# Kernel tuning notes

Hardware: AMD Instinct MI355X
Metric: run time of the kernel (lower is better)

## Reference

```python
import jax, jax.numpy as jnp
import numpy as np

FEATURES = 4096
BATCH = 2048


def setup_inputs() -> dict:
    key = jax.random.key(0)
    kx, kk = jax.random.split(key)
    x = jax.random.normal(kx, (BATCH, FEATURES), dtype=jnp.float32)
    kernel = jax.random.normal(kk, (FEATURES,), dtype=jnp.float32)
    return {"x": x, "kernel": kernel}


def reference(x, kernel):
    n = kernel.shape[0]
    i = jnp.arange(n)[:, None]   # [n,1]
    j = jnp.arange(n)[None, :]   # [1,n]
    idx = i - j                   # Toeplitz offsets
    # W[i,j] = kernel[i-j] if i>=j else 0  (causal lower-triangular Toeplitz)
    W = jnp.where(idx >= 0, kernel[jnp.clip(idx, 0, n - 1)], 0.0)
    # out[b,i] = sum_{j<=i} x[b,j] * kernel[i-j]  == x @ W.T
    return x @ W.T
```

## Files before the change

kernel.cpp:

```cpp
#include <hip/hip_runtime.h>
#include <hip/hip_bf16.h>


typedef unsigned short u16;
typedef __attribute__((ext_vector_type(8))) short  bf16x8;
typedef __attribute__((ext_vector_type(8))) unsigned short u16x8;
typedef __attribute__((ext_vector_type(4))) float  f32x4;

#define KDIM 4096
#define NDIM 4096
#define MDIM 2048
#define KREV_STRIDE 4608
#define KREV_BYTES  (8 * KREV_STRIDE * 2)
#define BSTRIDE 520

static __device__ inline u16 f2bf(float f) {
  unsigned u = __builtin_bit_cast(unsigned, f);
  unsigned r = u + 0x7FFFu + ((u >> 16) & 1u);
  return (u16)(r >> 16);
}

static __device__ inline void async_copy16(const void* g, void* l) {
  __builtin_amdgcn_global_load_lds((const __attribute__((address_space(1))) void*)g,
                                   (__attribute__((address_space(3))) void*)l,
                                   16, 0, 0);
}

__global__ __launch_bounds__(256) void prep(const float* __restrict__ x,
                                            const float* __restrict__ kern,
                                            u16* __restrict__ xb,
                                            u16* __restrict__ krevs,
                                            int conv_blocks) {
  int kb = (int)blockIdx.x - conv_blocks;
  if (kb >= 0) {
    int u = kb * 256 + threadIdx.x;
    for (int a = 0; a < 8; ++a) {
      int t = u + a - 8;
      u16 v = 0;
      if (t >= 0 && t <= 4095) v = f2bf(kern[4095 - t]);
      krevs[a * KREV_STRIDE + u] = v;
    }
  } else {
    size_t i = ((size_t)blockIdx.x * 256 + threadIdx.x) * 8;
    const f32x4* p = (const f32x4*)(x + i);
    f32x4 v0 = p[0], v1 = p[1];
    u16x8 r;
    r[0] = f2bf(v0[0]); r[1] = f2bf(v0[1]); r[2] = f2bf(v0[2]); r[3] = f2bf(v0[3]);
    r[4] = f2bf(v1[0]); r[5] = f2bf(v1[1]); r[6] = f2bf(v1[2]); r[7] = f2bf(v1[3]);
    *(u16x8*)(xb + i) = r;
  }
}

template <bool CONV>
__global__ __launch_bounds__(512, 4) void toeplitz_gemm(const void* __restrict__ Av,
                                                        const u16* __restrict__ krevs,
                                                        float* __restrict__ out) {
  __shared__ __align__(16) char smem_raw[49408];
  u16*   A_all = (u16*)smem_raw;
  u16*   B_all = (u16*)(smem_raw + 32768);
  f32x4* ep    = (f32x4*)smem_raw;

  const int tid  = threadIdx.x;
  const int w    = tid >> 6;
  const int g    = w >> 2;
  const int wl   = w & 3;
  const int lane = tid & 63;
  const int lane16 = lane & 15;
  const int quad   = lane >> 4;
  const int wm = wl >> 1;
  const int wn = wl & 1;

  const int b    = (int)blockIdx.x;
  const int rank = (b < 256) ? b : 511 - (b & 255);
  const int ct   = 31 - (rank >> 4);
  const int n0   = ct * 128;
  const int m0   = (rank & 15) * 128;
  const int W    = 3968 - n0;

  int boff[4];
  for (int fn = 0; fn < 4; ++fn) {
    int n_g = n0 + wn * 64 + fn * 16 + lane16;
    int s0  = 4095 - n_g + quad * 8;
    int a   = s0 & 7;
    boff[fn] = a * BSTRIDE + (s0 - a + 8 - W);
  }

  f32x4 acc[4][4] = {};
  const int srow8 = lane >> 3;
  const int ssrc  = ((lane & 7) ^ srow8) * 8;

  const u16*  xb = (const u16*)Av;
  const float* xf = (const float*)Av;
  u16* A_g = A_all + g * 8192;

  auto stageA = [&](int t) {
    const int k0 = t * 128 + g * 64;
    if constexpr (CONV) {
      int j    = tid & 255;
      int row  = j >> 1;
      int lh   = j & 1;
      for (int lc = 0; lc < 4; ++lc) {
        int l = lh * 4 + lc;
        int p = l ^ (row & 7);
        const f32x4* px = (const f32x4*)(xf + (size_t)(m0 + row) * KDIM + k0 + l * 8);
        f32x4 v0 = px[0], v1 = px[1];
        u16x8 r;
        r[0]=f2bf(v0[0]); r[1]=f2bf(v0[1]); r[2]=f2bf(v0[2]); r[3]=f2bf(v0[3]);
        r[4]=f2bf(v1[0]); r[5]=f2bf(v1[1]); r[6]=f2bf(v1[2]); r[7]=f2bf(v1[3]);
        *(u16x8*)(&A_g[row * 64 + p * 8]) = r;
      }
    } else {
      for (int c = 0; c < 4; ++c) {
        int g8  = c * 4 + wl;
        int row = g8 * 8 + srow8;
        async_copy16(xb + (size_t)(m0 + row) * KDIM + k0 + ssrc,
                     &A_g[g8 * 512]);
      }
    }
  };
  auto stageB = [&](int c) {
    async_copy16(krevs + w * KREV_STRIDE + W + c * 256 + (lane << 3),
                 &B_all[(c & 1) * 4160 + w * BSTRIDE]);
  };

  stageB(0);
  stageA(0);

  const int cmax = ct >> 1;
  for (int t = 0; ; ++t) {
    __syncthreads();
    const u16* Bb  = B_all + ((t >> 1) & 1) * 4160;
    const int  ksl = (t & 1) * 128 + g * 64;
    for (int kk = 0; kk < 2; ++kk) {
      bf16x8 af[4];
      const int p = (kk * 4 + quad) ^ (lane16 & 7);
      for (int fm = 0; fm < 4; ++fm) {
        int row = wm * 64 + fm * 16 + lane16;
        af[fm] = *(const bf16x8*)(&A_g[row * 64 + p * 8]);
      }
      bf16x8 bf[4];
      for (int fn = 0; fn < 4; ++fn)
        bf[fn] = *(const bf16x8*)(&Bb[boff[fn] + ksl + kk * 32]);
      for (int fm = 0; fm < 4; ++fm)
        for (int fn = 0; fn < 4; ++fn)
          acc[fm][fn] = __builtin_amdgcn_mfma_f32_16x16x32_bf16(af[fm], bf[fn], acc[fm][fn], 0, 0, 0);
    }
    if (t == ct) break;
    __syncthreads();
    stageA(t + 1);
    if (!(t & 1) && ((t >> 1) + 1) <= cmax) stageB((t >> 1) + 1);
  }

  const int j = tid & 255;
  for (int r = 0; r < 2; ++r) {
    __syncthreads();
    if (g == 1) {
      for (int fm2 = 0; fm2 < 2; ++fm2)
        for (int fn = 0; fn < 4; ++fn)
          ep[j * 9 + fm2 * 4 + fn] = acc[r * 2 + fm2][fn];
    }
    __syncthreads();
    if (g == 0) {
      for (int fm2 = 0; fm2 < 2; ++fm2)
        for (int fn = 0; fn < 4; ++fn)
          acc[r * 2 + fm2][fn] += ep[j * 9 + fm2 * 4 + fn];
    }
  }

  if (g == 0) {
    for (int fm = 0; fm < 4; ++fm) {
      int row_base = m0 + wm * 64 + fm * 16 + quad * 4;
      for (int fn = 0; fn < 4; ++fn) {
        int col = n0 + wn * 64 + fn * 16 + lane16;
        for (int r = 0; r < 4; ++r)
          out[(size_t)(row_base + r) * NDIM + col] = acc[fm][fn][r];
      }
    }
  }
}

extern "C" void kernel_launch(void* const* d_in, const int* in_sizes, int n_in,
                              void* d_out, int out_size, void* d_ws, size_t ws_size,
                              hipStream_t stream) {
  const float* x    = (const float*)d_in[0];
  const float* kern = (const float*)d_in[1];
  float* out = (float*)d_out;

  u16* krevs = (u16*)d_ws;
  u16* xb    = (u16*)((char*)d_ws + KREV_BYTES);
  const size_t need_fast = (size_t)KREV_BYTES + (size_t)MDIM * KDIM * 2;

  if (ws_size >= need_fast) {
    prep<<<4096 + 18, 256, 0, stream>>>(x, kern, xb, krevs, 4096);
    toeplitz_gemm<false><<<512, 512, 0, stream>>>(xb, krevs, out);
  } else {
    prep<<<18, 256, 0, stream>>>(x, kern, xb, krevs, 0);
    toeplitz_gemm<true><<<512, 512, 0, stream>>>(x, krevs, out);
  }
}
```

Baseline: 125.9 us.

## Split K across four wave groups with larger per-wave tiles and drop double buffering

The block now splits the K dimension four ways across wave pairs instead of two ways across groups of four waves. Each wave computes a 128x64 tile with 32 accumulators, so it reads more A fragments per B fragment. The prefetch double-buffering of A and B is removed: every iteration loads, syncs, then computes, and a two-stage LDS reduction combines the four partial sums. This aims to increase MFMA work per LDS read and per barrier. In exchange it doubles accumulator registers, lowers occupancy to 2 blocks per CU, and loses load/compute overlap.

```diff
diff --git a/kernel.cpp b/kernel.cpp
--- a/kernel.cpp
+++ b/kernel.cpp
@@ -52,23 +52,20 @@
 }
 
 template <bool CONV>
-__global__ __launch_bounds__(512, 4) void toeplitz_gemm(const void* __restrict__ Av,
+__global__ __launch_bounds__(512, 2) void toeplitz_gemm(const void* __restrict__ Av,
                                                         const u16* __restrict__ krevs,
                                                         float* __restrict__ out) {
-  __shared__ __align__(16) char smem_raw[49408];
-  u16*   A_all = (u16*)smem_raw;
-  u16*   B_all = (u16*)(smem_raw + 32768);
-  f32x4* ep    = (f32x4*)smem_raw;
+  __shared__ __align__(16) char smem[73856];
+  u16* A_all = (u16*)smem;
+  u16* B_all = (u16*)(smem + 65536);
 
   const int tid  = threadIdx.x;
   const int w    = tid >> 6;
-  const int g    = w >> 2;
-  const int wl   = w & 3;
+  const int g    = w >> 1;
+  const int wn2  = w & 1;
   const int lane = tid & 63;
   const int lane16 = lane & 15;
   const int quad   = lane >> 4;
-  const int wm = wl >> 1;
-  const int wn = wl & 1;
 
   const int b    = (int)blockIdx.x;
   const int rank = (b < 256) ? b : 511 - (b & 255);
@@ -79,13 +76,17 @@
 
   int boff[4];
   for (int fn = 0; fn < 4; ++fn) {
-    int n_g = n0 + wn * 64 + fn * 16 + lane16;
+    int n_g = n0 + wn2 * 64 + fn * 16 + lane16;
     int s0  = 4095 - n_g + quad * 8;
     int a   = s0 & 7;
     boff[fn] = a * BSTRIDE + (s0 - a + 8 - W);
   }
 
-  f32x4 acc[4][4] = {};
+  f32x4 acc[8][4] = {};
+
+  const int nk    = 2 * ct + 2;
+  const int iters = (nk + 3) >> 2;
+
   const int srow8 = lane >> 3;
   const int ssrc  = ((lane & 7) ^ srow8) * 8;
 
@@ -93,85 +94,71 @@
   const float* xf = (const float*)Av;
   u16* A_g = A_all + g * 8192;
 
-  auto stageA = [&](int t) {
-    const int k0 = t * 128 + g * 64;
-    if constexpr (CONV) {
-      int j    = tid & 255;
-      int row  = j >> 1;
-      int lh   = j & 1;
-      for (int lc = 0; lc < 4; ++lc) {
-        int l = lh * 4 + lc;
-        int p = l ^ (row & 7);
-        const f32x4* px = (const f32x4*)(xf + (size_t)(m0 + row) * KDIM + k0 + l * 8);
-        f32x4 v0 = px[0], v1 = px[1];
-        u16x8 r;
-        r[0]=f2bf(v0[0]); r[1]=f2bf(v0[1]); r[2]=f2bf(v0[2]); r[3]=f2bf(v0[3]);
-        r[4]=f2bf(v1[0]); r[5]=f2bf(v1[1]); r[6]=f2bf(v1[2]); r[7]=f2bf(v1[3]);
-        *(u16x8*)(&A_g[row * 64 + p * 8]) = r;
-      }
-    } else {
-      for (int c = 0; c < 4; ++c) {
-        int g8  = c * 4 + wl;
-        int row = g8 * 8 + srow8;
-        async_copy16(xb + (size_t)(m0 + row) * KDIM + k0 + ssrc,
-                     &A_g[g8 * 512]);
+  for (int t = 0; t < iters; ++t) {
+    const bool active = (4 * t + g) < nk;
+    const int  k0 = t * 256 + g * 64;
+    __syncthreads();
+    async_copy16(krevs + w * KREV_STRIDE + W + t * 256 + (lane << 3),
+                 &B_all[w * BSTRIDE]);
+    if (active) {
+      if constexpr (CONV) {
+        int row = tid & 127;
+        for (int c = 0; c < 8; ++c) {
+          int p = c ^ (row & 7);
+          const f32x4* px = (const f32x4*)(xf + (size_t)(m0 + row) * KDIM + k0 + c * 8);
+          f32x4 v0 = px[0], v1 = px[1];
+          u16x8 r;
+          r[0]=f2bf(v0[0]); r[1]=f2bf(v0[1]); r[2]=f2bf(v0[2]); r[3]=f2bf(v0[3]);
+          r[4]=f2bf(v1[0]); r[5]=f2bf(v1[1]); r[6]=f2bf(v1[2]); r[7]=f2bf(v1[3]);
+          *(u16x8*)(&A_g[row * 64 + p * 8]) = r;
+        }
+      } else {
+        for (int i = 0; i < 8; ++i) {
+          int base_row = wn2 * 64 + i * 8;
+          async_copy16(xb + (size_t)(m0 + base_row + srow8) * KDIM + k0 + ssrc,
+                       &A_g[base_row * 64]);
+        }
       }
     }
-  };
-  auto stageB = [&](int c) {
-    async_copy16(krevs + w * KREV_STRIDE + W + c * 256 + (lane << 3),
-                 &B_all[(c & 1) * 4160 + w * BSTRIDE]);
-  };
-
-  stageB(0);
-  stageA(0);
-
-  const int cmax = ct >> 1;
-  for (int t = 0; ; ++t) {
     __syncthreads();
-    const u16* Bb  = B_all + ((t >> 1) & 1) * 4160;
-    const int  ksl = (t & 1) * 128 + g * 64;
-    for (int kk = 0; kk < 2; ++kk) {
-      bf16x8 af[4];
-      const int p = (kk * 4 + quad) ^ (lane16 & 7);
-      for (int fm = 0; fm < 4; ++fm) {
-        int row = wm * 64 + fm * 16 + lane16;
-        af[fm] = *(const bf16x8*)(&A_g[row * 64 + p * 8]);
+    if (active) {
+      for (int kk = 0; kk < 2; ++kk) {
+        bf16x8 af[8];
+        const int p = (kk * 4 + quad) ^ (lane16 & 7);
+        for (int fm = 0; fm < 8; ++fm)
+          af[fm] = *(const bf16x8*)(&A_g[(fm * 16 + lane16) * 64 + p * 8]);
+        bf16x8 bf[4];
+        for (int fn = 0; fn < 4; ++fn)
+          bf[fn] = *(const bf16x8*)(&B_all[boff[fn] + g * 64 + kk * 32]);
+        for (int fm = 0; fm < 8; ++fm)
+          for (int fn = 0; fn < 4; ++fn)
+            acc[fm][fn] = __builtin_amdgcn_mfma_f32_16x16x32_bf16(af[fm], bf[fn], acc[fm][fn], 0, 0, 0);
       }
-      bf16x8 bf[4];
-      for (int fn = 0; fn < 4; ++fn)
-        bf[fn] = *(const bf16x8*)(&Bb[boff[fn] + ksl + kk * 32]);
-      for (int fm = 0; fm < 4; ++fm)
-        for (int fn = 0; fn < 4; ++fn)
-          acc[fm][fn] = __builtin_amdgcn_mfma_f32_16x16x32_bf16(af[fm], bf[fn], acc[fm][fn], 0, 0, 0);
-    }
-    if (t == ct) break;
-    __syncthreads();
-    stageA(t + 1);
-    if (!(t & 1) && ((t >> 1) + 1) <= cmax) stageB((t >> 1) + 1);
-  }
-
-  const int j = tid & 255;
-  for (int r = 0; r < 2; ++r) {
-    __syncthreads();
-    if (g == 1) {
-      for (int fm2 = 0; fm2 < 2; ++fm2)
-        for (int fn = 0; fn < 4; ++fn)
-          ep[j * 9 + fm2 * 4 + fn] = acc[r * 2 + fm2][fn];
-    }
-    __syncthreads();
-    if (g == 0) {
-      for (int fm2 = 0; fm2 < 2; ++fm2)
-        for (int fn = 0; fn < 4; ++fn)
-          acc[r * 2 + fm2][fn] += ep[j * 9 + fm2 * 4 + fn];
     }
   }
 
+  auto xchg = [&](bool writer, bool reader, int pr) {
+    for (int r = 0; r < 2; ++r) {
+      __syncthreads();
+      if (writer)
+        for (int f = 0; f < 16; ++f)
+          *(f32x4*)(smem + pr * 34816 + wn2 * 17408 + f * 1088 + lane * 16) =
+              acc[r * 4 + (f >> 2)][f & 3];
+      __syncthreads();
+      if (reader)
+        for (int f = 0; f < 16; ++f)
+          acc[r * 4 + (f >> 2)][f & 3] +=
+              *(const f32x4*)(smem + pr * 34816 + wn2 * 17408 + f * 1088 + lane * 16);
+    }
+  };
+  xchg(g == 1 || g == 3, g == 0 || g == 2, g >> 1);
+  xchg(g == 2, g == 0, 0);
+
   if (g == 0) {
-    for (int fm = 0; fm < 4; ++fm) {
-      int row_base = m0 + wm * 64 + fm * 16 + quad * 4;
+    for (int fm = 0; fm < 8; ++fm) {
+      int row_base = m0 + fm * 16 + quad * 4;
       for (int fn = 0; fn < 4; ++fn) {
-        int col = n0 + wn * 64 + fn * 16 + lane16;
+        int col = n0 + wn2 * 64 + fn * 16 + lane16;
         for (int r = 0; r < 4; ++r)
           out[(size_t)(row_base + r) * NDIM + col] = acc[fm][fn][r];
       }
```

Result: slower. 136.2 us (+8.2%).

## Split-K the long causal Toeplitz tiles and reduce partials in a separate kernel

Applied to the files above, without the earlier changes.

Adds a split-K mode in which the 256 output tiles with the longest K ranges (column tiles 16-31) are each split into two halves that compute partial sums. Those partials are written to workspace and summed by a new reduce kernel. Blocks are ordered so that each group of 80 pairs heavy split halves with lighter unsplit tiles, balancing load across 768 blocks instead of 512. The aim is to remove the long tail from triangular work imbalance, at the cost of an extra 32 MB of partial traffic and an additional kernel launch.

```diff
diff --git a/kernel.cpp b/kernel.cpp
--- a/kernel.cpp
+++ b/kernel.cpp
@@ -13,6 +13,8 @@
 #define KREV_STRIDE 4608
 #define KREV_BYTES  (8 * KREV_STRIDE * 2)
 #define BSTRIDE 520
+#define XB_BYTES  (MDIM * KDIM * 2)
+#define PART_BYTES (2 * 256 * 16384 * 4)
 
 static __device__ inline u16 f2bf(float f) {
   unsigned u = __builtin_bit_cast(unsigned, f);
@@ -51,10 +53,32 @@
   }
 }
 
+__global__ __launch_bounds__(256) void reduce_parts(const float* __restrict__ partials,
+                                                    float* __restrict__ out) {
+  const int rb = (int)blockIdx.x;
+  const int tileIdx = rb >> 1;
+  const int hh = rb & 1;
+  const int ct = 16 + (tileIdx >> 4);
+  const int mt = tileIdx & 15;
+  const f32x4* p0 = (const f32x4*)(partials + (size_t)tileIdx * 16384);
+  const f32x4* p1 = (const f32x4*)(partials + (size_t)(256 + tileIdx) * 16384);
+  for (int i = 0; i < 8; ++i) {
+    int chunk = hh * 2048 + (int)threadIdx.x + i * 256;
+    int row = chunk >> 5;
+    int c4  = chunk & 31;
+    f32x4 v = p0[chunk];
+    f32x4 w = p1[chunk];
+    v[0]+=w[0]; v[1]+=w[1]; v[2]+=w[2]; v[3]+=w[3];
+    *(f32x4*)(out + (size_t)(mt * 128 + row) * NDIM + ct * 128 + c4 * 4) = v;
+  }
+}
+
 template <bool CONV>
 __global__ __launch_bounds__(512, 4) void toeplitz_gemm(const void* __restrict__ Av,
                                                         const u16* __restrict__ krevs,
-                                                        float* __restrict__ out) {
+                                                        float* __restrict__ out,
+                                                        float* __restrict__ partials,
+                                                        int split_mode) {
   __shared__ __align__(16) char smem_raw[49408];
   u16*   A_all = (u16*)smem_raw;
   u16*   B_all = (u16*)(smem_raw + 32768);
@@ -70,19 +94,35 @@
   const int wm = wl >> 1;
   const int wn = wl & 1;
 
-  const int b    = (int)blockIdx.x;
-  const int rank = (b < 256) ? b : 511 - (b & 255);
-  const int ct   = 31 - (rank >> 4);
-  const int n0   = ct * 128;
-  const int m0   = (rank & 15) * 128;
-  const int W    = 3968 - n0;
+  int ct, mt, s0, cnt, h = 0, split = 0;
+  const int b = (int)blockIdx.x;
+  if (split_mode) {
+    if (b < 640) {
+      int p = b / 80, r = b % 80;
+      if (r < 48) {
+        if (r < 32) { split = 1; ct = 31 - 2 * p; h = r >> 4; mt = r & 15; }
+        else        { split = 0; ct = 15 - p;     mt = r - 32; }
+      } else        { split = 1; ct = 30 - 2 * p; int r2 = r - 48; h = r2 >> 4; mt = r2 & 15; }
+    } else {
+      int j = b - 640; split = 0; ct = 7 - (j >> 4); mt = j & 15;
+    }
+  } else {
+    const int rank = (b < 256) ? b : 511 - (b & 255);
+    ct = 31 - (rank >> 4); mt = rank & 15;
+  }
+  if (split) { s0 = h * (ct + 1); cnt = ct + 1; }
+  else       { s0 = 0;            cnt = 2 * ct + 2; }
+
+  const int n0 = ct * 128;
+  const int m0 = mt * 128;
+  const int W  = 3968 - n0;
 
   int boff[4];
   for (int fn = 0; fn < 4; ++fn) {
     int n_g = n0 + wn * 64 + fn * 16 + lane16;
-    int s0  = 4095 - n_g + quad * 8;
-    int a   = s0 & 7;
-    boff[fn] = a * BSTRIDE + (s0 - a + 8 - W);
+    int s0f = 4095 - n_g + quad * 8;
+    int a   = s0f & 7;
+    boff[fn] = a * BSTRIDE + (s0f - a + 8 - W);
   }
 
   f32x4 acc[4][4] = {};
@@ -93,8 +133,8 @@
   const float* xf = (const float*)Av;
   u16* A_g = A_all + g * 8192;
 
-  auto stageA = [&](int t) {
-    const int k0 = t * 128 + g * 64;
+  auto stageA = [&](int ls) {
+    const int k0 = (s0 + ls) * 64;
     if constexpr (CONV) {
       int j    = tid & 255;
       int row  = j >> 1;
@@ -119,36 +159,40 @@
     }
   };
   auto stageB = [&](int c) {
-    async_copy16(krevs + w * KREV_STRIDE + W + c * 256 + (lane << 3),
+    async_copy16(krevs + w * KREV_STRIDE + W + s0 * 64 + c * 256 + (lane << 3),
                  &B_all[(c & 1) * 4160 + w * BSTRIDE]);
   };
 
+  const int T   = (cnt + 1) >> 1;
+  const int nch = (T + 1) >> 1;
+
   stageB(0);
-  stageA(0);
-
-  const int cmax = ct >> 1;
-  for (int t = 0; ; ++t) {
-    __syncthreads();
-    const u16* Bb  = B_all + ((t >> 1) & 1) * 4160;
-    const int  ksl = (t & 1) * 128 + g * 64;
-    for (int kk = 0; kk < 2; ++kk) {
-      bf16x8 af[4];
-      const int p = (kk * 4 + quad) ^ (lane16 & 7);
-      for (int fm = 0; fm < 4; ++fm) {
-        int row = wm * 64 + fm * 16 + lane16;
-        af[fm] = *(const bf16x8*)(&A_g[row * 64 + p * 8]);
-      }
-      bf16x8 bf[4];
-      for (int fn = 0; fn < 4; ++fn)
-        bf[fn] = *(const bf16x8*)(&Bb[boff[fn] + ksl + kk * 32]);
-      for (int fm = 0; fm < 4; ++fm)
+  stageA(g);
+
+  for (int t = 0;; ++t) {
+    __syncthreads();
+    if (2 * t + g < cnt) {
+      const u16* Bb  = B_all + ((t >> 1) & 1) * 4160;
+      const int  ksl = (t & 1) * 128 + g * 64;
+      for (int kk = 0; kk < 2; ++kk) {
+        bf16x8 af[4];
+        const int p = (kk * 4 + quad) ^ (lane16 & 7);
+        for (int fm = 0; fm < 4; ++fm) {
+          int row = wm * 64 + fm * 16 + lane16;
+          af[fm] = *(const bf16x8*)(&A_g[row * 64 + p * 8]);
+        }
+        bf16x8 bf[4];
         for (int fn = 0; fn < 4; ++fn)
-          acc[fm][fn] = __builtin_amdgcn_mfma_f32_16x16x32_bf16(af[fm], bf[fn], acc[fm][fn], 0, 0, 0);
-    }
-    if (t == ct) break;
-    __syncthreads();
-    stageA(t + 1);
-    if (!(t & 1) && ((t >> 1) + 1) <= cmax) stageB((t >> 1) + 1);
+          bf[fn] = *(const bf16x8*)(&Bb[boff[fn] + ksl + kk * 32]);
+        for (int fm = 0; fm < 4; ++fm)
+          for (int fn = 0; fn < 4; ++fn)
+            acc[fm][fn] = __builtin_amdgcn_mfma_f32_16x16x32_bf16(af[fm], bf[fn], acc[fm][fn], 0, 0, 0);
+      }
+    }
+    if (t + 1 == T) break;
+    __syncthreads();
+    if (2 * (t + 1) + g < cnt) stageA(2 * (t + 1) + g);
+    if (!(t & 1) && (t >> 1) + 1 < nch) stageB((t >> 1) + 1);
   }
 
   const int j = tid & 255;
@@ -168,12 +212,24 @@
   }
 
   if (g == 0) {
-    for (int fm = 0; fm < 4; ++fm) {
-      int row_base = m0 + wm * 64 + fm * 16 + quad * 4;
-      for (int fn = 0; fn < 4; ++fn) {
-        int col = n0 + wn * 64 + fn * 16 + lane16;
-        for (int r = 0; r < 4; ++r)
-          out[(size_t)(row_base + r) * NDIM + col] = acc[fm][fn][r];
+    if (split) {
+      float* pp = partials + (size_t)(h * 256 + (ct - 16) * 16 + mt) * 16384;
+      for (int fm = 0; fm < 4; ++fm) {
+        int rl = wm * 64 + fm * 16 + quad * 4;
+        for (int fn = 0; fn < 4; ++fn) {
+          int cl = wn * 64 + fn * 16 + lane16;
+          for (int r = 0; r < 4; ++r)
+            pp[(rl + r) * 128 + cl] = acc[fm][fn][r];
+        }
+      }
+    } else {
+      for (int fm = 0; fm < 4; ++fm) {
+        int row_base = m0 + wm * 64 + fm * 16 + quad * 4;
+        for (int fn = 0; fn < 4; ++fn) {
+          int col = n0 + wn * 64 + fn * 16 + lane16;
+          for (int r = 0; r < 4; ++r)
+            out[(size_t)(row_base + r) * NDIM + col] = acc[fm][fn][r];
+        }
       }
     }
   }
@@ -186,15 +242,22 @@
   const float* kern = (const float*)d_in[1];
   float* out = (float*)d_out;
 
-  u16* krevs = (u16*)d_ws;
-  u16* xb    = (u16*)((char*)d_ws + KREV_BYTES);
-  const size_t need_fast = (size_t)KREV_BYTES + (size_t)MDIM * KDIM * 2;
-
-  if (ws_size >= need_fast) {
+  u16*   krevs    = (u16*)d_ws;
+  u16*   xb       = (u16*)((char*)d_ws + KREV_BYTES);
+  float* partials = (float*)((char*)d_ws + KREV_BYTES + XB_BYTES);
+
+  const size_t need_fast  = (size_t)KREV_BYTES + XB_BYTES;
+  const size_t need_split = need_fast + PART_BYTES;
+
+  if (ws_size >= need_split) {
     prep<<<4096 + 18, 256, 0, stream>>>(x, kern, xb, krevs, 4096);
-    toeplitz_gemm<false><<<512, 512, 0, stream>>>(xb, krevs, out);
+    toeplitz_gemm<false><<<768, 512, 0, stream>>>(xb, krevs, out, partials, 1);
+    reduce_parts<<<512, 256, 0, stream>>>(partials, out);
+  } else if (ws_size >= need_fast) {
+    prep<<<4096 + 18, 256, 0, stream>>>(x, kern, xb, krevs, 4096);
+    toeplitz_gemm<false><<<512, 512, 0, stream>>>(xb, krevs, out, partials, 0);
   } else {
     prep<<<18, 256, 0, stream>>>(x, kern, xb, krevs, 0);
-    toeplitz_gemm<true><<<512, 512, 0, stream>>>(x, krevs, out);
-  }
-}
+    toeplitz_gemm<true><<<512, 512, 0, stream>>>(x, krevs, out, partials, 0);
+  }
+}
```

New measurement: 127.9 us. Within noise of the previous version (+1.6%).
